# Kernel tuning notes

Measured on AMD Instinct MI355X. Metric: run time of the kernel, lower is better.

Reference implementation:

```python
import jax, jax.numpy as jnp
import numpy as np
import math

# B queries, N complex ambient dim, M codebook entries, S payload dim, K quad nodes
B, N, M, S, K = 1024, 128, 8192, 256, 8
EPS_TOTAL = 1e-3
OVERLAP, ANISO = 0.25, 0.75
_t, _w = np.polynomial.hermite.hermgauss(K)
GH_T = jnp.asarray(_t, jnp.float32)
GH_W = jnp.asarray(_w, jnp.float32)


def _init_sigmas():
    # mirrors CPSFFusedCodebook._init_sigmas (log-space for numerical safety at N=128)
    rho = 1.0 + ANISO
    logV = (N / 2.0) * math.log(math.pi) - math.lgamma(N / 2.0 + 1.0)
    log_r = (math.log(OVERLAP) - math.log(M) - logV - math.log(rho)) / N
    r_perp = math.exp(log_r)
    s_perp = 2.0 * math.pi * r_perp ** 2
    return rho * rho * s_perp, s_perp


def setup_inputs() -> dict:
    key = jax.random.key(0)
    ks = jax.random.split(key, 12)
    u = lambda k, sh: jax.random.uniform(k, sh, jnp.float32, -1.0, 1.0)
    s_par, s_perp = _init_sigmas()
    return {
        "z_re": u(ks[0], (B, N)), "z_im": u(ks[1], (B, N)),
        "d_re": u(ks[2], (B, N)), "d_im": u(ks[3], (B, N)),
        "zj_re": 0.5 * u(ks[4], (M, N)), "zj_im": 0.5 * u(ks[5], (M, N)),
        "dj_re": 0.5 * u(ks[6], (M, N)), "dj_im": 0.5 * u(ks[7], (M, N)),
        "T_re": u(ks[8], (M, S)), "T_im": u(ks[9], (M, S)),
        "alpha": jax.random.uniform(ks[10], (M,), jnp.float32, 0.5, 1.5),
        "sigma_par": jnp.full((M,), s_par, jnp.float32),
        "sigma_perp": jnp.full((M,), s_perp, jnp.float32),
    }


def _unit(xr, xi):
    n = jnp.sqrt(jnp.sum(xr * xr + xi * xi, -1, keepdims=True))
    n = jnp.where(n == 0, jnp.ones_like(n), n)
    return xr / n, xi / n


def _forward(z_re, z_im, d_re, d_im, zj_re, zj_im, dj_re, dj_im,
             T_re, T_im, alpha, sigma_par, sigma_perp):
    tiny = jnp.float32(np.finfo(np.float32).tiny)
    dur, dui = _unit(d_re, d_im)          # autonorm_vec_d
    djr, dji = _unit(dj_re, dj_im)        # autonorm_vec_d_j
    a = jnp.maximum(alpha, tiny)
    sp = jnp.maximum(sigma_par, tiny)
    sq = jnp.maximum(sigma_perp, tiny)

    # proj[b,m] = <d_j, z - z_j> (conj-linear in d_j); all via GEMMs, no [B,M,N] tensor
    pr = z_re @ djr.T + z_im @ dji.T - jnp.sum(djr * zj_re + dji * zj_im, -1)[None, :]
    pi = z_im @ djr.T - z_re @ dji.T - jnp.sum(djr * zj_im - dji * zj_re, -1)[None, :]

    # |z - z_j|^2 via GEMM expansion
    dz2 = (jnp.sum(z_re * z_re + z_im * z_im, -1)[:, None]
           + jnp.sum(zj_re * zj_re + zj_im * zj_im, -1)[None, :]
           - 2.0 * (z_re @ zj_re.T + z_im @ zj_im.T))
    perp2 = jnp.maximum(dz2 - (pr * pr + pi * pi), 0.0)  # component orthogonal to d_j

    # Gauss-Hermite quadrature along the codebook direction, scaled per-code
    scale = jnp.sqrt(sp / jnp.pi)                     # [M]
    t = GH_T[None, :] * scale[:, None]                # [M,K] quad offsets
    par2 = (pr[:, :, None] - t[None]) ** 2 + (pi * pi)[:, :, None]   # [B,M,K]
    env = jnp.exp(-jnp.pi * (par2 / sp[None, :, None]
                             + (perp2 / sq[None, :])[:, :, None]))
    rho = jnp.einsum('bmk,k->bm', env, GH_W) * (scale / jnp.sqrt(jnp.pi))[None, :]

    # angular alignment |<d_j, d>|^2
    ar = dur @ djr.T + dui @ dji.T
    ai = dui @ djr.T - dur @ dji.T
    align = ar * ar + ai * ai

    w = a[None, :] * align * rho                      # [B,M] real mixture weights
    den = jnp.sum(w, -1) + EPS_TOTAL                  # [B]
    out_re = (w @ T_re) / den[:, None]                # [B,S]
    out_im = (w @ T_im) / den[:, None]
    return jnp.stack([out_re, out_im], -1)            # [B,S,2] == complex [B,S]


def reference(z_re, z_im, d_re, d_im, zj_re, zj_im, dj_re, dj_im,
              T_re, T_im, alpha, sigma_par, sigma_perp):
    return _forward(z_re, z_im, d_re, d_im, zj_re, zj_im, dj_re, dj_im,
                    T_re, T_im, alpha, sigma_par, sigma_perp)
```

## Files before the change

### kernel.cpp

```cpp
#include <hip/hip_runtime.h>
#include <math.h>

#define Bq 1024
#define Nn 128
#define Mm 8192
#define Ss 256

typedef _Float16 f16;
typedef _Float16 f16x8 __attribute__((ext_vector_type(8)));
typedef _Float16 f16x4 __attribute__((ext_vector_type(4)));
typedef float f32x4 __attribute__((ext_vector_type(4)));

#define PI_F 3.14159265358979323846f
#define INV_SQRT_PI 0.5641895835477563f
#define TINY_F 1.17549435e-38f
#define EPS_TOTAL 1e-3f
#define WSC 1024.0f

#define GLOAD16(g, l) \
    __builtin_amdgcn_global_load_lds((const __attribute__((address_space(1))) void*)(g), \
                                     (__attribute__((address_space(3))) void*)(l), 16, 0, 0)

__global__ void cpsf_prep_b(const float* __restrict__ z_re, const float* __restrict__ z_im,
                            const float* __restrict__ d_re, const float* __restrict__ d_im,
                            float* __restrict__ z2, float* __restrict__ invd)
{
    const int b = blockIdx.x * 4 + (threadIdx.x >> 6);
    const int l = threadIdx.x & 63;
    const int o = b * Nn;
    float dr0 = d_re[o + l], dr1 = d_re[o + l + 64];
    float di0 = d_im[o + l], di1 = d_im[o + l + 64];
    float zr0 = z_re[o + l], zr1 = z_re[o + l + 64];
    float zi0 = z_im[o + l], zi1 = z_im[o + l + 64];
    float sd = dr0*dr0 + di0*di0 + dr1*dr1 + di1*di1;
    float sz = zr0*zr0 + zi0*zi0 + zr1*zr1 + zi1*zi1;
#pragma unroll
    for (int off = 1; off < 64; off <<= 1) {
        sd += __shfl_xor(sd, off);
        sz += __shfl_xor(sz, off);
    }
    if (l == 0) {
        float nd = sqrtf(sd);
        nd = (nd == 0.0f) ? 1.0f : nd;
        z2[b] = sz;
        invd[b] = 1.0f / nd;
    }
}

__global__ void cpsf_prep_m(const float* __restrict__ zj_re, const float* __restrict__ zj_im,
                            const float* __restrict__ dj_re, const float* __restrict__ dj_im,
                            const float* __restrict__ alpha, const float* __restrict__ sp_,
                            const float* __restrict__ sq_, float* __restrict__ cm)
{
    const int m = blockIdx.x * 4 + (threadIdx.x >> 6);
    const int l = threadIdx.x & 63;
    const int o = m * Nn;
    float dr0 = dj_re[o + l], dr1 = dj_re[o + l + 64];
    float di0 = dj_im[o + l], di1 = dj_im[o + l + 64];
    float zr0 = zj_re[o + l], zr1 = zj_re[o + l + 64];
    float zi0 = zj_im[o + l], zi1 = zj_im[o + l + 64];
    float snd = dr0*dr0 + di0*di0 + dr1*dr1 + di1*di1;
    float sc1 = dr0*zr0 + di0*zi0 + dr1*zr1 + di1*zi1;
    float sc2 = dr0*zi0 - di0*zr0 + dr1*zi1 - di1*zr1;
    float sz2 = zr0*zr0 + zi0*zi0 + zr1*zr1 + zi1*zi1;
#pragma unroll
    for (int off = 1; off < 64; off <<= 1) {
        snd += __shfl_xor(snd, off);
        sc1 += __shfl_xor(sc1, off);
        sc2 += __shfl_xor(sc2, off);
        sz2 += __shfl_xor(sz2, off);
    }
    if (l == 0) {
        float nd = sqrtf(snd);
        nd = (nd == 0.0f) ? 1.0f : nd;
        float inv = 1.0f / nd;
        cm[0*Mm + m] = inv;
        cm[1*Mm + m] = sc1 * inv;
        cm[2*Mm + m] = sc2 * inv;
        cm[3*Mm + m] = sz2;
        float sp = fmaxf(sp_[m], TINY_F);
        float sq = fmaxf(sq_[m], TINY_F);
        float sc = sqrtf(sp / PI_F);
        cm[4*Mm + m] = PI_F / sp;
        cm[5*Mm + m] = PI_F / sq;
        cm[6*Mm + m] = fmaxf(alpha[m], TINY_F) * sc * INV_SQRT_PI;
        cm[7*Mm + m] = sc;
    }
}

__global__ void cpsf_pack_ab(const float* __restrict__ z_re, const float* __restrict__ z_im,
                             const float* __restrict__ d_re, const float* __restrict__ d_im,
                             const float* __restrict__ invd, f16* __restrict__ Az, f16* __restrict__ Au)
{
    int idx = blockIdx.x * 256 + threadIdx.x;
    int b = idx >> 6, k4 = (idx & 63) * 4;
    float4 vz, vd;
    if (k4 < 128) {
        vz = *(const float4*)(z_re + b * Nn + k4);
        vd = *(const float4*)(d_re + b * Nn + k4);
    } else {
        vz = *(const float4*)(z_im + b * Nn + k4 - 128);
        vd = *(const float4*)(d_im + b * Nn + k4 - 128);
    }
    float s = invd[b];
    *(f16x4*)(Az + b * 256 + k4) = (f16x4){(f16)vz.x, (f16)vz.y, (f16)vz.z, (f16)vz.w};
    *(f16x4*)(Au + b * 256 + k4) = (f16x4){(f16)(vd.x*s), (f16)(vd.y*s), (f16)(vd.z*s), (f16)(vd.w*s)};
}

__global__ void cpsf_pack_b1(const float* __restrict__ zj_re, const float* __restrict__ zj_im,
                             const float* __restrict__ dj_re, const float* __restrict__ dj_im,
                             const float* __restrict__ cm, f16* __restrict__ Bp,
                             int Mc, int m0g, int mshift)
{
    int idx = blockIdx.x * 256 + threadIdx.x;
    int r = idx >> 6, k4 = (idx & 63) * 4;
    int p = r >> mshift, ml = r & (Mc - 1);
    int m = m0g + ml;
    float4 v; float s;
    if (p == 0) {
        v = (k4 < 128) ? *(const float4*)(dj_re + m * Nn + k4)
                       : *(const float4*)(dj_im + m * Nn + k4 - 128);
        s = cm[m];
    } else if (p == 1) {
        if (k4 < 128) { v = *(const float4*)(dj_im + m * Nn + k4); v.x=-v.x; v.y=-v.y; v.z=-v.z; v.w=-v.w; }
        else          { v = *(const float4*)(dj_re + m * Nn + k4 - 128); }
        s = cm[m];
    } else {
        v = (k4 < 128) ? *(const float4*)(zj_re + m * Nn + k4)
                       : *(const float4*)(zj_im + m * Nn + k4 - 128);
        s = 1.0f;
    }
    *(f16x4*)(Bp + (size_t)r * 256 + k4) = (f16x4){(f16)(v.x*s), (f16)(v.y*s), (f16)(v.z*s), (f16)(v.w*s)};
}

__global__ void cpsf_pack_tt(const float* __restrict__ T_re, const float* __restrict__ T_im,
                             f16* __restrict__ Tt, int Mc, int m0g)
{
    __shared__ float tr[64][65], ti[64][65];
    const int mb = blockIdx.x * 64, sb = blockIdx.y * 64;
    const int tid = threadIdx.x;
    const int i0 = tid >> 6, j = tid & 63;
#pragma unroll
    for (int it = 0; it < 16; ++it) {
        int i = it * 4 + i0;
        tr[i][j] = T_re[(size_t)(m0g + mb + i) * Ss + sb + j];
        ti[i][j] = T_im[(size_t)(m0g + mb + i) * Ss + sb + j];
    }
    __syncthreads();
#pragma unroll
    for (int it = 0; it < 16; ++it) {
        int jj = it * 4 + i0;
        int sp = (sb + jj) * 2;
        Tt[(size_t)sp * Mc + mb + j]       = (f16)tr[j][jj];
        Tt[(size_t)(sp + 1) * Mc + mb + j] = (f16)ti[j][jj];
    }
}

__global__ __launch_bounds__(256, 2) void cpsf_gemm_w(
    const f16* __restrict__ Az, const f16* __restrict__ Au,
    const f16* __restrict__ Bp, const float* __restrict__ cm,
    const float* __restrict__ z2v, f16* __restrict__ wbuf,
    float* __restrict__ den, int Mc, int m0g)
{
    __shared__ __align__(16) f16 sm[1792 * 8];

    const int tid = threadIdx.x;
    const int wid = tid >> 6;
    const int lane = tid & 63;
    const int q = lane >> 4;
    const int li = lane & 15;
    const int mb0 = blockIdx.x * 64;
    const int bb0 = blockIdx.y * 128;
    const int wb0 = (wid >> 1) * 64;
    const int wm0 = (wid & 1) * 32;

    const f16* gp[7];
    f16* lb[7];
#pragma unroll
    for (int i = 0; i < 7; ++i) {
        int c = i * 4 + wid;
        const f16* src;
        if (c < 8) {
            int g = c >> 1, row = (c & 1) * 64 + lane;
            src = Az + (size_t)(bb0 + row) * 256 + g * 8;
        } else if (c < 16) {
            int c2 = c - 8;
            int g = c2 >> 1, row = (c2 & 1) * 64 + lane;
            src = Au + (size_t)(bb0 + row) * 256 + g * 8;
        } else {
            int c2 = c - 16;
            int g = c2 / 3, p = c2 % 3;
            src = Bp + ((size_t)p * Mc + mb0 + lane) * 256 + g * 8;
        }
        gp[i] = src;
        lb[i] = sm + (size_t)(i * 256 + wid * 64) * 8;
    }

    f32x4 accP[4][2][3];
    f32x4 accQ[4][2][2];
#pragma unroll
    for (int t = 0; t < 4; ++t)
#pragma unroll
        for (int u = 0; u < 2; ++u) {
#pragma unroll
            for (int p = 0; p < 3; ++p) accP[t][u][p] = (f32x4){0.f,0.f,0.f,0.f};
#pragma unroll
            for (int p = 0; p < 2; ++p) accQ[t][u][p] = (f32x4){0.f,0.f,0.f,0.f};
        }

    for (int ks = 0; ks < 8; ++ks) {
        __syncthreads();
#pragma unroll
        for (int i = 0; i < 7; ++i) {
            GLOAD16(gp[i], lb[i]);
            gp[i] += 32;
        }
        __syncthreads();

        f16x8 az[4], au[4], bf[3][2];
#pragma unroll
        for (int t = 0; t < 4; ++t) {
            az[t] = *(const f16x8*)(sm + (size_t)(q * 128 + wb0 + t * 16 + li) * 8);
            au[t] = *(const f16x8*)(sm + (size_t)(512 + q * 128 + wb0 + t * 16 + li) * 8);
        }
#pragma unroll
        for (int p = 0; p < 3; ++p)
#pragma unroll
            for (int u = 0; u < 2; ++u)
                bf[p][u] = *(const f16x8*)(sm + (size_t)(1024 + q * 192 + p * 64 + wm0 + u * 16 + li) * 8);

#pragma unroll
        for (int t = 0; t < 4; ++t)
#pragma unroll
            for (int u = 0; u < 2; ++u) {
#pragma unroll
                for (int p = 0; p < 3; ++p)
                    accP[t][u][p] = __builtin_amdgcn_mfma_f32_16x16x32_f16(az[t], bf[p][u], accP[t][u][p], 0, 0, 0);
#pragma unroll
                for (int p = 0; p < 2; ++p)
                    accQ[t][u][p] = __builtin_amdgcn_mfma_f32_16x16x32_f16(au[t], bf[p][u], accQ[t][u][p], 0, 0, 0);
            }
    }

    const float GT[8] = {-2.9306374202572440f, -1.9816567566958429f,
                         -1.1571937124467802f, -0.3811869902073221f,
                          0.3811869902073221f,  1.1571937124467802f,
                          1.9816567566958429f,  2.9306374202572440f};
    const float GW[8] = {1.9960407221136762e-04f, 1.7077983007413475e-02f,
                         2.0780232581489188e-01f, 6.6114701255824129e-01f,
                         6.6114701255824129e-01f, 2.0780232581489188e-01f,
                         1.7077983007413475e-02f, 1.9960407221136762e-04f};

    float c1[2], c2[2], zj2[2], isp[2], isq[2], cf[2], scl[2];
#pragma unroll
    for (int u = 0; u < 2; ++u) {
        int mg = m0g + mb0 + wm0 + u * 16 + li;
        c1[u]  = cm[1*Mm + mg];  c2[u]  = cm[2*Mm + mg];
        zj2[u] = cm[3*Mm + mg];  isp[u] = cm[4*Mm + mg];
        isq[u] = cm[5*Mm + mg];  cf[u]  = cm[6*Mm + mg];
        scl[u] = cm[7*Mm + mg];
    }

    float dsum[4][4];
#pragma unroll
    for (int t = 0; t < 4; ++t)
#pragma unroll
        for (int r = 0; r < 4; ++r) dsum[t][r] = 0.f;

#pragma unroll
    for (int t = 0; t < 4; ++t) {
#pragma unroll
        for (int r = 0; r < 4; ++r) {
            const int b = bb0 + wb0 + t * 16 + q * 4 + r;
            const float z2b = z2v[b];
#pragma unroll
            for (int u = 0; u < 2; ++u) {
                float pr = accP[t][u][0][r] - c1[u];
                float pi = accP[t][u][1][r] - c2[u];
                float dz2 = z2b + zj2[u] - 2.0f * accP[t][u][2][r];
                float perp2 = fmaxf(dz2 - pr * pr - pi * pi, 0.0f);
                float base = -(isq[u] * perp2 + isp[u] * pi * pi);
                float rho = 0.0f;
#pragma unroll
                for (int k = 0; k < 8; ++k) {
                    float dd = pr - scl[u] * GT[k];
                    rho = fmaf(GW[k], __expf(base - isp[u] * dd * dd), rho);
                }
                float ar = accQ[t][u][0][r], ai = accQ[t][u][1][r];
                float wv = cf[u] * (ar * ar + ai * ai) * rho;
                dsum[t][r] += wv;
                wbuf[(size_t)b * Mc + mb0 + wm0 + u * 16 + li] = (f16)(wv * WSC);
            }
        }
    }
#pragma unroll
    for (int t = 0; t < 4; ++t)
#pragma unroll
        for (int r = 0; r < 4; ++r) {
            float v = dsum[t][r];
            v += __shfl_xor(v, 1);
            v += __shfl_xor(v, 2);
            v += __shfl_xor(v, 4);
            v += __shfl_xor(v, 8);
            if (li == 0) atomicAdd(den + bb0 + wb0 + t * 16 + q * 4 + r, v);
        }
}

__global__ __launch_bounds__(256, 3) void cpsf_gemm_out(
    const f16* __restrict__ wbuf, const f16* __restrict__ Tt,
    float* __restrict__ oacc, int Mc, int Kw)
{
    __shared__ __align__(16) f16 sm[1024 * 8];
    const int tid = threadIdx.x;
    const int wid = tid >> 6;
    const int lane = tid & 63;
    const int q = lane >> 4;
    const int li = lane & 15;
    const int sb0 = blockIdx.x * 128;
    const int bb0 = blockIdx.y * 128;
    const int kz0 = blockIdx.z * Kw;
    const int wb0 = (wid >> 1) * 64;
    const int ws0 = (wid & 1) * 64;

    const f16* gp[4];
    f16* lb[4];
#pragma unroll
    for (int i = 0; i < 4; ++i) {
        int c = i * 4 + wid;
        const f16* src;
        if (c < 8) {
            int g = c >> 1, row = (c & 1) * 64 + lane;
            src = wbuf + (size_t)(bb0 + row) * Mc + kz0 + g * 8;
        } else {
            int c2 = c - 8;
            int g = c2 >> 1, row = (c2 & 1) * 64 + lane;
            src = Tt + (size_t)(sb0 + row) * Mc + kz0 + g * 8;
        }
        gp[i] = src;
        lb[i] = sm + (size_t)(i * 256 + wid * 64) * 8;
    }

    f32x4 acc[4][4];
#pragma unroll
    for (int t = 0; t < 4; ++t)
#pragma unroll
        for (int u = 0; u < 4; ++u) acc[t][u] = (f32x4){0.f,0.f,0.f,0.f};

    for (int kc = 0; kc < Kw; kc += 32) {
        __syncthreads();
#pragma unroll
        for (int i = 0; i < 4; ++i) {
            GLOAD16(gp[i], lb[i]);
            gp[i] += 32;
        }
        __syncthreads();
        f16x8 af[4], bf[4];
#pragma unroll
        for (int t = 0; t < 4; ++t)
            af[t] = *(const f16x8*)(sm + (size_t)(q * 128 + wb0 + t * 16 + li) * 8);
#pragma unroll
        for (int u = 0; u < 4; ++u)
            bf[u] = *(const f16x8*)(sm + (size_t)(512 + q * 128 + ws0 + u * 16 + li) * 8);
#pragma unroll
        for (int t = 0; t < 4; ++t)
#pragma unroll
            for (int u = 0; u < 4; ++u)
                acc[t][u] = __builtin_amdgcn_mfma_f32_16x16x32_f16(af[t], bf[u], acc[t][u], 0, 0, 0);
    }
#pragma unroll
    for (int t = 0; t < 4; ++t)
#pragma unroll
        for (int u = 0; u < 4; ++u)
#pragma unroll
            for (int r = 0; r < 4; ++r)
                atomicAdd(oacc + (size_t)(bb0 + wb0 + t * 16 + q * 4 + r) * 512 + sb0 + ws0 + u * 16 + li,
                          acc[t][u][r]);
}

__global__ void cpsf_fin(const float* __restrict__ oacc, const float* __restrict__ den,
                         float* __restrict__ out)
{
    int i = blockIdx.x * 256 + threadIdx.x;
    float d = (den[i >> 9] + EPS_TOTAL) * WSC;
    out[i] = oacc[i] / d;
}

extern "C" void kernel_launch(void* const* d_in, const int* in_sizes, int n_in,
                              void* d_out, int out_size, void* d_ws, size_t ws_size,
                              hipStream_t stream)
{
    (void)in_sizes; (void)n_in; (void)out_size;
    const float* z_re  = (const float*)d_in[0];
    const float* z_im  = (const float*)d_in[1];
    const float* d_re  = (const float*)d_in[2];
    const float* d_im  = (const float*)d_in[3];
    const float* zj_re = (const float*)d_in[4];
    const float* zj_im = (const float*)d_in[5];
    const float* dj_re = (const float*)d_in[6];
    const float* dj_im = (const float*)d_in[7];
    const float* T_re  = (const float*)d_in[8];
    const float* T_im  = (const float*)d_in[9];
    const float* alpha = (const float*)d_in[10];
    const float* s_par = (const float*)d_in[11];
    const float* s_perp= (const float*)d_in[12];

    char* w8 = (char*)d_ws;
    const size_t o_out  = 0;
    const size_t o_den  = o_out + (size_t)Bq * 512 * 4;
    const size_t o_z2   = o_den + 4096;
    const size_t o_invd = o_z2 + 4096;
    const size_t o_cm   = o_invd + 4096;
    const size_t o_az   = o_cm + (size_t)8 * Mm * 4;
    const size_t o_au   = o_az + (size_t)Bq * 256 * 2;
    const size_t o_ch   = o_au + (size_t)Bq * 256 * 2;
    int Mc = 512;
    if      (o_ch + (size_t)4608 * 8192 <= ws_size) Mc = 8192;
    else if (o_ch + (size_t)4608 * 4096 <= ws_size) Mc = 4096;
    else if (o_ch + (size_t)4608 * 2048 <= ws_size) Mc = 2048;
    else if (o_ch + (size_t)4608 * 1024 <= ws_size) Mc = 1024;
    int mshift = 31 - __builtin_clz((unsigned)Mc);
    int zs = Mc / 1024; if (zs < 1) zs = 1;
    int Kw = Mc / zs;

    float* oacc = (float*)(w8 + o_out);
    float* den  = (float*)(w8 + o_den);
    float* z2   = (float*)(w8 + o_z2);
    float* invd = (float*)(w8 + o_invd);
    float* cm   = (float*)(w8 + o_cm);
    f16*   Az   = (f16*)(w8 + o_az);
    f16*   Au   = (f16*)(w8 + o_au);
    f16*   Bp   = (f16*)(w8 + o_ch);
    f16*   Tt   = (f16*)(w8 + o_ch + (size_t)1536 * Mc);
    f16*   wb   = (f16*)(w8 + o_ch + (size_t)2560 * Mc);

    hipMemsetAsync(d_ws, 0, o_z2, stream);

    cpsf_prep_b<<<Bq / 4, 256, 0, stream>>>(z_re, z_im, d_re, d_im, z2, invd);
    cpsf_prep_m<<<Mm / 4, 256, 0, stream>>>(zj_re, zj_im, dj_re, dj_im, alpha, s_par, s_perp, cm);
    cpsf_pack_ab<<<(Bq * 64) / 256, 256, 0, stream>>>(z_re, z_im, d_re, d_im, invd, Az, Au);

    for (int m0 = 0; m0 < Mm; m0 += Mc) {
        cpsf_pack_b1<<<(3 * Mc * 64) / 256, 256, 0, stream>>>(zj_re, zj_im, dj_re, dj_im,
                                                              cm, Bp, Mc, m0, mshift);
        cpsf_pack_tt<<<dim3(Mc / 64, Ss / 64), 256, 0, stream>>>(T_re, T_im, Tt, Mc, m0);
        cpsf_gemm_w<<<dim3(Mc / 64, Bq / 128), 256, 0, stream>>>(Az, Au, Bp, cm, z2, wb, den, Mc, m0);
        cpsf_gemm_out<<<dim3(4, Bq / 128, zs), 256, 0, stream>>>(wb, Tt, oacc, Mc, Kw);
    }
    cpsf_fin<<<(Bq * 512) / 256, 256, 0, stream>>>(oacc, den, (float*)d_out);
}
```

Before: 247.9 us.

## Split alignment GEMM into separate kernel to shrink gemm_w register pressure

```diff
diff --git a/kernel.cpp b/kernel.cpp
--- a/kernel.cpp
+++ b/kernel.cpp
@@ -156,13 +156,93 @@
     }
 }
 
+__global__ __launch_bounds__(256, 2) void cpsf_align(
+    const f16* __restrict__ Au, const f16* __restrict__ Bp,
+    f16* __restrict__ wbuf, int Mc)
+{
+    __shared__ __align__(16) f16 sm[1536 * 8];
+
+    const int tid = threadIdx.x;
+    const int wid = tid >> 6;
+    const int lane = tid & 63;
+    const int q = lane >> 4;
+    const int li = lane & 15;
+    const int mb0 = blockIdx.x * 128;
+    const int bb0 = blockIdx.y * 128;
+    const int wb0 = (wid >> 1) * 64;
+    const int wm0 = (wid & 1) * 64;
+
+    const f16* gp[6];
+    f16* lb[6];
+#pragma unroll
+    for (int i = 0; i < 6; ++i) {
+        int c = i * 4 + wid;
+        const f16* src;
+        if (c < 8) {
+            int g = c >> 1, row = (c & 1) * 64 + lane;
+            src = Au + (size_t)(bb0 + row) * 256 + g * 8;
+        } else {
+            int c2 = c - 8;
+            int g = c2 >> 2, p = (c2 >> 1) & 1, row = (c2 & 1) * 64 + lane;
+            src = Bp + ((size_t)p * Mc + mb0 + row) * 256 + g * 8;
+        }
+        gp[i] = src;
+        lb[i] = sm + (size_t)(i * 4 + wid) * 64 * 8;
+    }
+
+    f32x4 acc[4][4][2];
+#pragma unroll
+    for (int t = 0; t < 4; ++t)
+#pragma unroll
+        for (int u = 0; u < 4; ++u) {
+            acc[t][u][0] = (f32x4){0.f,0.f,0.f,0.f};
+            acc[t][u][1] = (f32x4){0.f,0.f,0.f,0.f};
+        }
+
+    for (int ks = 0; ks < 8; ++ks) {
+        __syncthreads();
+#pragma unroll
+        for (int i = 0; i < 6; ++i) {
+            GLOAD16(gp[i], lb[i]);
+            gp[i] += 32;
+        }
+        __syncthreads();
+        f16x8 au[4], bf[2][4];
+#pragma unroll
+        for (int t = 0; t < 4; ++t)
+            au[t] = *(const f16x8*)(sm + (size_t)(q * 128 + wb0 + t * 16 + li) * 8);
+#pragma unroll
+        for (int p = 0; p < 2; ++p)
+#pragma unroll
+            for (int u = 0; u < 4; ++u)
+                bf[p][u] = *(const f16x8*)(sm + (size_t)(512 + q * 256 + p * 128 + wm0 + u * 16 + li) * 8);
+#pragma unroll
+        for (int t = 0; t < 4; ++t)
+#pragma unroll
+            for (int u = 0; u < 4; ++u) {
+                acc[t][u][0] = __builtin_amdgcn_mfma_f32_16x16x32_f16(au[t], bf[0][u], acc[t][u][0], 0, 0, 0);
+                acc[t][u][1] = __builtin_amdgcn_mfma_f32_16x16x32_f16(au[t], bf[1][u], acc[t][u][1], 0, 0, 0);
+            }
+    }
+#pragma unroll
+    for (int t = 0; t < 4; ++t)
+#pragma unroll
+        for (int u = 0; u < 4; ++u)
+#pragma unroll
+            for (int r = 0; r < 4; ++r) {
+                int b = bb0 + wb0 + t * 16 + q * 4 + r;
+                int m = mb0 + wm0 + u * 16 + li;
+                float ar = acc[t][u][0][r], ai = acc[t][u][1][r];
+                wbuf[(size_t)b * Mc + m] = (f16)(ar * ar + ai * ai);
+            }
+}
+
 __global__ __launch_bounds__(256, 2) void cpsf_gemm_w(
-    const f16* __restrict__ Az, const f16* __restrict__ Au,
-    const f16* __restrict__ Bp, const float* __restrict__ cm,
-    const float* __restrict__ z2v, f16* __restrict__ wbuf,
-    float* __restrict__ den, int Mc, int m0g)
-{
-    __shared__ __align__(16) f16 sm[1792 * 8];
+    const f16* __restrict__ Az, const f16* __restrict__ Bp,
+    const float* __restrict__ cm, const float* __restrict__ z2v,
+    f16* __restrict__ wbuf, float* __restrict__ den, int Mc, int m0g)
+{
+    __shared__ __align__(16) f16 sm[1280 * 8];
 
     const int tid = threadIdx.x;
     const int wid = tid >> 6;
@@ -174,72 +254,56 @@
     const int wb0 = (wid >> 1) * 64;
     const int wm0 = (wid & 1) * 32;
 
-    const f16* gp[7];
-    f16* lb[7];
-#pragma unroll
-    for (int i = 0; i < 7; ++i) {
+    const f16* gp[5];
+    f16* lb[5];
+#pragma unroll
+    for (int i = 0; i < 5; ++i) {
         int c = i * 4 + wid;
         const f16* src;
         if (c < 8) {
             int g = c >> 1, row = (c & 1) * 64 + lane;
             src = Az + (size_t)(bb0 + row) * 256 + g * 8;
-        } else if (c < 16) {
+        } else {
             int c2 = c - 8;
-            int g = c2 >> 1, row = (c2 & 1) * 64 + lane;
-            src = Au + (size_t)(bb0 + row) * 256 + g * 8;
-        } else {
-            int c2 = c - 16;
             int g = c2 / 3, p = c2 % 3;
             src = Bp + ((size_t)p * Mc + mb0 + lane) * 256 + g * 8;
         }
         gp[i] = src;
-        lb[i] = sm + (size_t)(i * 256 + wid * 64) * 8;
+        lb[i] = sm + (size_t)(i * 4 + wid) * 64 * 8;
     }
 
     f32x4 accP[4][2][3];
-    f32x4 accQ[4][2][2];
-#pragma unroll
-    for (int t = 0; t < 4; ++t)
-#pragma unroll
-        for (int u = 0; u < 2; ++u) {
+#pragma unroll
+    for (int t = 0; t < 4; ++t)
+#pragma unroll
+        for (int u = 0; u < 2; ++u)
 #pragma unroll
             for (int p = 0; p < 3; ++p) accP[t][u][p] = (f32x4){0.f,0.f,0.f,0.f};
-#pragma unroll
-            for (int p = 0; p < 2; ++p) accQ[t][u][p] = (f32x4){0.f,0.f,0.f,0.f};
-        }
 
     for (int ks = 0; ks < 8; ++ks) {
         __syncthreads();
 #pragma unroll
-        for (int i = 0; i < 7; ++i) {
+        for (int i = 0; i < 5; ++i) {
             GLOAD16(gp[i], lb[i]);
             gp[i] += 32;
         }
         __syncthreads();
-
-        f16x8 az[4], au[4], bf[3][2];
-#pragma unroll
-        for (int t = 0; t < 4; ++t) {
+        f16x8 az[4], bf[3][2];
+#pragma unroll
+        for (int t = 0; t < 4; ++t)
             az[t] = *(const f16x8*)(sm + (size_t)(q * 128 + wb0 + t * 16 + li) * 8);
-            au[t] = *(const f16x8*)(sm + (size_t)(512 + q * 128 + wb0 + t * 16 + li) * 8);
-        }
 #pragma unroll
         for (int p = 0; p < 3; ++p)
 #pragma unroll
             for (int u = 0; u < 2; ++u)
-                bf[p][u] = *(const f16x8*)(sm + (size_t)(1024 + q * 192 + p * 64 + wm0 + u * 16 + li) * 8);
-
+                bf[p][u] = *(const f16x8*)(sm + (size_t)(512 + q * 192 + p * 64 + wm0 + u * 16 + li) * 8);
 #pragma unroll
         for (int t = 0; t < 4; ++t)
 #pragma unroll
-            for (int u = 0; u < 2; ++u) {
+            for (int u = 0; u < 2; ++u)
 #pragma unroll
                 for (int p = 0; p < 3; ++p)
                     accP[t][u][p] = __builtin_amdgcn_mfma_f32_16x16x32_f16(az[t], bf[p][u], accP[t][u][p], 0, 0, 0);
-#pragma unroll
-                for (int p = 0; p < 2; ++p)
-                    accQ[t][u][p] = __builtin_amdgcn_mfma_f32_16x16x32_f16(au[t], bf[p][u], accQ[t][u][p], 0, 0, 0);
-            }
     }
 
     const float GT[8] = {-2.9306374202572440f, -1.9816567566958429f,
@@ -275,6 +339,8 @@
             const float z2b = z2v[b];
 #pragma unroll
             for (int u = 0; u < 2; ++u) {
+                const size_t widx = (size_t)b * Mc + mb0 + wm0 + u * 16 + li;
+                float al = (float)wbuf[widx];
                 float pr = accP[t][u][0][r] - c1[u];
                 float pi = accP[t][u][1][r] - c2[u];
                 float dz2 = z2b + zj2[u] - 2.0f * accP[t][u][2][r];
@@ -286,10 +352,9 @@
                     float dd = pr - scl[u] * GT[k];
                     rho = fmaf(GW[k], __expf(base - isp[u] * dd * dd), rho);
                 }
-                float ar = accQ[t][u][0][r], ai = accQ[t][u][1][r];
-                float wv = cf[u] * (ar * ar + ai * ai) * rho;
+                float wv = cf[u] * al * rho;
                 dsum[t][r] += wv;
-                wbuf[(size_t)b * Mc + mb0 + wm0 + u * 16 + li] = (f16)(wv * WSC);
+                wbuf[widx] = (f16)(wv * WSC);
             }
         }
     }
@@ -419,7 +484,7 @@
     else if (o_ch + (size_t)4608 * 2048 <= ws_size) Mc = 2048;
     else if (o_ch + (size_t)4608 * 1024 <= ws_size) Mc = 1024;
     int mshift = 31 - __builtin_clz((unsigned)Mc);
-    int zs = Mc / 1024; if (zs < 1) zs = 1;
+    int zs = Mc / 512; if (zs < 1) zs = 1;
     int Kw = Mc / zs;
 
     float* oacc = (float*)(w8 + o_out);
@@ -443,7 +508,8 @@
         cpsf_pack_b1<<<(3 * Mc * 64) / 256, 256, 0, stream>>>(zj_re, zj_im, dj_re, dj_im,
                                                               cm, Bp, Mc, m0, mshift);
         cpsf_pack_tt<<<dim3(Mc / 64, Ss / 64), 256, 0, stream>>>(T_re, T_im, Tt, Mc, m0);
-        cpsf_gemm_w<<<dim3(Mc / 64, Bq / 128), 256, 0, stream>>>(Az, Au, Bp, cm, z2, wb, den, Mc, m0);
+        cpsf_align<<<dim3(Mc / 128, Bq / 128), 256, 0, stream>>>(Au, Bp, wb, Mc);
+        cpsf_gemm_w<<<dim3(Mc / 64, Bq / 128), 256, 0, stream>>>(Az, Bp, cm, z2, wb, den, Mc, m0);
         cpsf_gemm_out<<<dim3(4, Bq / 128, zs), 256, 0, stream>>>(wb, Tt, oacc, Mc, Kw);
     }
     cpsf_fin<<<(Bq * 512) / 256, 256, 0, stream>>>(oacc, den, (float*)d_out);
```

Measured after the change: 275.0 us. +11.0%, slower.

## Fuse fp16 packing into prep kernels, drop M-chunking, retile both GEMMs

Applied to the files above, without the earlier changes.

```diff
diff --git a/kernel.cpp b/kernel.cpp
--- a/kernel.cpp
+++ b/kernel.cpp
@@ -8,7 +8,6 @@
 
 typedef _Float16 f16;
 typedef _Float16 f16x8 __attribute__((ext_vector_type(8)));
-typedef _Float16 f16x4 __attribute__((ext_vector_type(4)));
 typedef float f32x4 __attribute__((ext_vector_type(4)));
 
 #define PI_F 3.14159265358979323846f
@@ -21,9 +20,9 @@
     __builtin_amdgcn_global_load_lds((const __attribute__((address_space(1))) void*)(g), \
                                      (__attribute__((address_space(3))) void*)(l), 16, 0, 0)
 
-__global__ void cpsf_prep_b(const float* __restrict__ z_re, const float* __restrict__ z_im,
+__global__ void cpsf_prep_a(const float* __restrict__ z_re, const float* __restrict__ z_im,
                             const float* __restrict__ d_re, const float* __restrict__ d_im,
-                            float* __restrict__ z2, float* __restrict__ invd)
+                            float* __restrict__ z2, f16* __restrict__ Az, f16* __restrict__ Au)
 {
     const int b = blockIdx.x * 4 + (threadIdx.x >> 6);
     const int l = threadIdx.x & 63;
@@ -39,18 +38,22 @@
         sd += __shfl_xor(sd, off);
         sz += __shfl_xor(sz, off);
     }
-    if (l == 0) {
-        float nd = sqrtf(sd);
-        nd = (nd == 0.0f) ? 1.0f : nd;
-        z2[b] = sz;
-        invd[b] = 1.0f / nd;
-    }
+    float nd = sqrtf(sd);
+    nd = (nd == 0.0f) ? 1.0f : nd;
+    float inv = 1.0f / nd;
+    if (l == 0) z2[b] = sz;
+    const int o2 = b * 256;
+    Az[o2 + l]       = (f16)zr0;  Az[o2 + 64 + l]  = (f16)zr1;
+    Az[o2 + 128 + l] = (f16)zi0;  Az[o2 + 192 + l] = (f16)zi1;
+    Au[o2 + l]       = (f16)(dr0*inv);  Au[o2 + 64 + l]  = (f16)(dr1*inv);
+    Au[o2 + 128 + l] = (f16)(di0*inv);  Au[o2 + 192 + l] = (f16)(di1*inv);
 }
 
 __global__ void cpsf_prep_m(const float* __restrict__ zj_re, const float* __restrict__ zj_im,
                             const float* __restrict__ dj_re, const float* __restrict__ dj_im,
                             const float* __restrict__ alpha, const float* __restrict__ sp_,
-                            const float* __restrict__ sq_, float* __restrict__ cm)
+                            const float* __restrict__ sq_, float* __restrict__ cm,
+                            f16* __restrict__ Bp)
 {
     const int m = blockIdx.x * 4 + (threadIdx.x >> 6);
     const int l = threadIdx.x & 63;
@@ -70,11 +73,19 @@
         sc2 += __shfl_xor(sc2, off);
         sz2 += __shfl_xor(sz2, off);
     }
+    float nd = sqrtf(snd);
+    nd = (nd == 0.0f) ? 1.0f : nd;
+    float inv = 1.0f / nd;
+    const size_t b0o = (size_t)m * 256;
+    const size_t b1o = ((size_t)Mm + m) * 256;
+    const size_t b2o = ((size_t)2 * Mm + m) * 256;
+    Bp[b0o + l]       = (f16)(dr0*inv);  Bp[b0o + 64 + l]  = (f16)(dr1*inv);
+    Bp[b0o + 128 + l] = (f16)(di0*inv);  Bp[b0o + 192 + l] = (f16)(di1*inv);
+    Bp[b1o + l]       = (f16)(-di0*inv); Bp[b1o + 64 + l]  = (f16)(-di1*inv);
+    Bp[b1o + 128 + l] = (f16)(dr0*inv);  Bp[b1o + 192 + l] = (f16)(dr1*inv);
+    Bp[b2o + l]       = (f16)zr0;        Bp[b2o + 64 + l]  = (f16)zr1;
+    Bp[b2o + 128 + l] = (f16)zi0;        Bp[b2o + 192 + l] = (f16)zi1;
     if (l == 0) {
-        float nd = sqrtf(snd);
-        nd = (nd == 0.0f) ? 1.0f : nd;
-        float inv = 1.0f / nd;
-        cm[0*Mm + m] = inv;
         cm[1*Mm + m] = sc1 * inv;
         cm[2*Mm + m] = sc2 * inv;
         cm[3*Mm + m] = sz2;
@@ -88,53 +99,8 @@
     }
 }
 
-__global__ void cpsf_pack_ab(const float* __restrict__ z_re, const float* __restrict__ z_im,
-                             const float* __restrict__ d_re, const float* __restrict__ d_im,
-                             const float* __restrict__ invd, f16* __restrict__ Az, f16* __restrict__ Au)
-{
-    int idx = blockIdx.x * 256 + threadIdx.x;
-    int b = idx >> 6, k4 = (idx & 63) * 4;
-    float4 vz, vd;
-    if (k4 < 128) {
-        vz = *(const float4*)(z_re + b * Nn + k4);
-        vd = *(const float4*)(d_re + b * Nn + k4);
-    } else {
-        vz = *(const float4*)(z_im + b * Nn + k4 - 128);
-        vd = *(const float4*)(d_im + b * Nn + k4 - 128);
-    }
-    float s = invd[b];
-    *(f16x4*)(Az + b * 256 + k4) = (f16x4){(f16)vz.x, (f16)vz.y, (f16)vz.z, (f16)vz.w};
-    *(f16x4*)(Au + b * 256 + k4) = (f16x4){(f16)(vd.x*s), (f16)(vd.y*s), (f16)(vd.z*s), (f16)(vd.w*s)};
-}
-
-__global__ void cpsf_pack_b1(const float* __restrict__ zj_re, const float* __restrict__ zj_im,
-                             const float* __restrict__ dj_re, const float* __restrict__ dj_im,
-                             const float* __restrict__ cm, f16* __restrict__ Bp,
-                             int Mc, int m0g, int mshift)
-{
-    int idx = blockIdx.x * 256 + threadIdx.x;
-    int r = idx >> 6, k4 = (idx & 63) * 4;
-    int p = r >> mshift, ml = r & (Mc - 1);
-    int m = m0g + ml;
-    float4 v; float s;
-    if (p == 0) {
-        v = (k4 < 128) ? *(const float4*)(dj_re + m * Nn + k4)
-                       : *(const float4*)(dj_im + m * Nn + k4 - 128);
-        s = cm[m];
-    } else if (p == 1) {
-        if (k4 < 128) { v = *(const float4*)(dj_im + m * Nn + k4); v.x=-v.x; v.y=-v.y; v.z=-v.z; v.w=-v.w; }
-        else          { v = *(const float4*)(dj_re + m * Nn + k4 - 128); }
-        s = cm[m];
-    } else {
-        v = (k4 < 128) ? *(const float4*)(zj_re + m * Nn + k4)
-                       : *(const float4*)(zj_im + m * Nn + k4 - 128);
-        s = 1.0f;
-    }
-    *(f16x4*)(Bp + (size_t)r * 256 + k4) = (f16x4){(f16)(v.x*s), (f16)(v.y*s), (f16)(v.z*s), (f16)(v.w*s)};
-}
-
 __global__ void cpsf_pack_tt(const float* __restrict__ T_re, const float* __restrict__ T_im,
-                             f16* __restrict__ Tt, int Mc, int m0g)
+                             f16* __restrict__ Tt)
 {
     __shared__ float tr[64][65], ti[64][65];
     const int mb = blockIdx.x * 64, sb = blockIdx.y * 64;
@@ -143,26 +109,26 @@
 #pragma unroll
     for (int it = 0; it < 16; ++it) {
         int i = it * 4 + i0;
-        tr[i][j] = T_re[(size_t)(m0g + mb + i) * Ss + sb + j];
-        ti[i][j] = T_im[(size_t)(m0g + mb + i) * Ss + sb + j];
+        tr[i][j] = T_re[(size_t)(mb + i) * Ss + sb + j];
+        ti[i][j] = T_im[(size_t)(mb + i) * Ss + sb + j];
     }
     __syncthreads();
 #pragma unroll
     for (int it = 0; it < 16; ++it) {
         int jj = it * 4 + i0;
         int sp = (sb + jj) * 2;
-        Tt[(size_t)sp * Mc + mb + j]       = (f16)tr[j][jj];
-        Tt[(size_t)(sp + 1) * Mc + mb + j] = (f16)ti[j][jj];
-    }
-}
-
-__global__ __launch_bounds__(256, 2) void cpsf_gemm_w(
+        Tt[(size_t)sp * Mm + mb + j]       = (f16)tr[j][jj];
+        Tt[(size_t)(sp + 1) * Mm + mb + j] = (f16)ti[j][jj];
+    }
+}
+
+__global__ __launch_bounds__(256, 3) void cpsf_gemm_w(
     const f16* __restrict__ Az, const f16* __restrict__ Au,
     const f16* __restrict__ Bp, const float* __restrict__ cm,
     const float* __restrict__ z2v, f16* __restrict__ wbuf,
-    float* __restrict__ den, int Mc, int m0g)
-{
-    __shared__ __align__(16) f16 sm[1792 * 8];
+    float* __restrict__ den)
+{
+    __shared__ __align__(16) f16 sm[2560 * 8];
 
     const int tid = threadIdx.x;
     const int wid = tid >> 6;
@@ -170,36 +136,33 @@
     const int q = lane >> 4;
     const int li = lane & 15;
     const int mb0 = blockIdx.x * 64;
-    const int bb0 = blockIdx.y * 128;
-    const int wb0 = (wid >> 1) * 64;
+    const int bb0 = blockIdx.y * 64;
+    const int wb0 = (wid >> 1) * 32;
     const int wm0 = (wid & 1) * 32;
 
-    const f16* gp[7];
-    f16* lb[7];
-#pragma unroll
-    for (int i = 0; i < 7; ++i) {
+    const f16* gp[10];
+    f16* lb[10];
+#pragma unroll
+    for (int i = 0; i < 10; ++i) {
         int c = i * 4 + wid;
         const f16* src;
         if (c < 8) {
-            int g = c >> 1, row = (c & 1) * 64 + lane;
-            src = Az + (size_t)(bb0 + row) * 256 + g * 8;
+            src = Az + (size_t)(bb0 + lane) * 256 + c * 8;
         } else if (c < 16) {
-            int c2 = c - 8;
-            int g = c2 >> 1, row = (c2 & 1) * 64 + lane;
-            src = Au + (size_t)(bb0 + row) * 256 + g * 8;
+            int g = c - 8;
+            src = Au + (size_t)(bb0 + lane) * 256 + g * 8;
         } else {
-            int c2 = c - 16;
-            int g = c2 / 3, p = c2 % 3;
-            src = Bp + ((size_t)p * Mc + mb0 + lane) * 256 + g * 8;
+            int c2 = c - 16, g = c2 / 3, p = c2 % 3;
+            src = Bp + ((size_t)p * Mm + mb0 + lane) * 256 + g * 8;
         }
         gp[i] = src;
-        lb[i] = sm + (size_t)(i * 256 + wid * 64) * 8;
-    }
-
-    f32x4 accP[4][2][3];
-    f32x4 accQ[4][2][2];
-#pragma unroll
-    for (int t = 0; t < 4; ++t)
+        lb[i] = sm + (size_t)c * 64 * 8;
+    }
+
+    f32x4 accP[2][2][3];
+    f32x4 accQ[2][2][2];
+#pragma unroll
+    for (int t = 0; t < 2; ++t)
 #pragma unroll
         for (int u = 0; u < 2; ++u) {
 #pragma unroll
@@ -208,38 +171,39 @@
             for (int p = 0; p < 2; ++p) accQ[t][u][p] = (f32x4){0.f,0.f,0.f,0.f};
         }
 
-    for (int ks = 0; ks < 8; ++ks) {
+    for (int ks = 0; ks < 4; ++ks) {
         __syncthreads();
 #pragma unroll
-        for (int i = 0; i < 7; ++i) {
+        for (int i = 0; i < 10; ++i) {
             GLOAD16(gp[i], lb[i]);
-            gp[i] += 32;
+            gp[i] += 64;
         }
         __syncthreads();
-
-        f16x8 az[4], au[4], bf[3][2];
-#pragma unroll
-        for (int t = 0; t < 4; ++t) {
-            az[t] = *(const f16x8*)(sm + (size_t)(q * 128 + wb0 + t * 16 + li) * 8);
-            au[t] = *(const f16x8*)(sm + (size_t)(512 + q * 128 + wb0 + t * 16 + li) * 8);
-        }
-#pragma unroll
-        for (int p = 0; p < 3; ++p)
-#pragma unroll
-            for (int u = 0; u < 2; ++u)
-                bf[p][u] = *(const f16x8*)(sm + (size_t)(1024 + q * 192 + p * 64 + wm0 + u * 16 + li) * 8);
-
-#pragma unroll
-        for (int t = 0; t < 4; ++t)
-#pragma unroll
-            for (int u = 0; u < 2; ++u) {
-#pragma unroll
-                for (int p = 0; p < 3; ++p)
-                    accP[t][u][p] = __builtin_amdgcn_mfma_f32_16x16x32_f16(az[t], bf[p][u], accP[t][u][p], 0, 0, 0);
-#pragma unroll
-                for (int p = 0; p < 2; ++p)
-                    accQ[t][u][p] = __builtin_amdgcn_mfma_f32_16x16x32_f16(au[t], bf[p][u], accQ[t][u][p], 0, 0, 0);
+#pragma unroll
+        for (int j = 0; j < 2; ++j) {
+            const int g = j * 4 + q;
+            f16x8 az[2], au[2], bf[3][2];
+#pragma unroll
+            for (int t = 0; t < 2; ++t) {
+                az[t] = *(const f16x8*)(sm + (size_t)(g * 64 + wb0 + t * 16 + li) * 8);
+                au[t] = *(const f16x8*)(sm + (size_t)(512 + g * 64 + wb0 + t * 16 + li) * 8);
             }
+#pragma unroll
+            for (int p = 0; p < 3; ++p)
+#pragma unroll
+                for (int u = 0; u < 2; ++u)
+                    bf[p][u] = *(const f16x8*)(sm + (size_t)(1024 + (g * 3 + p) * 64 + wm0 + u * 16 + li) * 8);
+#pragma unroll
+            for (int t = 0; t < 2; ++t)
+#pragma unroll
+                for (int u = 0; u < 2; ++u) {
+#pragma unroll
+                    for (int p = 0; p < 3; ++p)
+                        accP[t][u][p] = __builtin_amdgcn_mfma_f32_16x16x32_f16(az[t], bf[p][u], accP[t][u][p], 0, 0, 0);
+                    accQ[t][u][0] = __builtin_amdgcn_mfma_f32_16x16x32_f16(au[t], bf[0][u], accQ[t][u][0], 0, 0, 0);
+                    accQ[t][u][1] = __builtin_amdgcn_mfma_f32_16x16x32_f16(au[t], bf[1][u], accQ[t][u][1], 0, 0, 0);
+                }
+        }
     }
 
     const float GT[8] = {-2.9306374202572440f, -1.9816567566958429f,
@@ -254,21 +218,21 @@
     float c1[2], c2[2], zj2[2], isp[2], isq[2], cf[2], scl[2];
 #pragma unroll
     for (int u = 0; u < 2; ++u) {
-        int mg = m0g + mb0 + wm0 + u * 16 + li;
+        int mg = mb0 + wm0 + u * 16 + li;
         c1[u]  = cm[1*Mm + mg];  c2[u]  = cm[2*Mm + mg];
         zj2[u] = cm[3*Mm + mg];  isp[u] = cm[4*Mm + mg];
         isq[u] = cm[5*Mm + mg];  cf[u]  = cm[6*Mm + mg];
         scl[u] = cm[7*Mm + mg];
     }
 
-    float dsum[4][4];
-#pragma unroll
-    for (int t = 0; t < 4; ++t)
+    float dsum[2][4];
+#pragma unroll
+    for (int t = 0; t < 2; ++t)
 #pragma unroll
         for (int r = 0; r < 4; ++r) dsum[t][r] = 0.f;
 
 #pragma unroll
-    for (int t = 0; t < 4; ++t) {
+    for (int t = 0; t < 2; ++t) {
 #pragma unroll
         for (int r = 0; r < 4; ++r) {
             const int b = bb0 + wb0 + t * 16 + q * 4 + r;
@@ -289,12 +253,12 @@
                 float ar = accQ[t][u][0][r], ai = accQ[t][u][1][r];
                 float wv = cf[u] * (ar * ar + ai * ai) * rho;
                 dsum[t][r] += wv;
-                wbuf[(size_t)b * Mc + mb0 + wm0 + u * 16 + li] = (f16)(wv * WSC);
+                wbuf[(size_t)b * Mm + mb0 + wm0 + u * 16 + li] = (f16)(wv * WSC);
             }
         }
     }
 #pragma unroll
-    for (int t = 0; t < 4; ++t)
+    for (int t = 0; t < 2; ++t)
 #pragma unroll
         for (int r = 0; r < 4; ++r) {
             float v = dsum[t][r];
@@ -306,69 +270,74 @@
         }
 }
 
-__global__ __launch_bounds__(256, 3) void cpsf_gemm_out(
+__global__ __launch_bounds__(256, 4) void cpsf_gemm_out(
     const f16* __restrict__ wbuf, const f16* __restrict__ Tt,
-    float* __restrict__ oacc, int Mc, int Kw)
-{
-    __shared__ __align__(16) f16 sm[1024 * 8];
+    float* __restrict__ oacc)
+{
+    __shared__ __align__(16) f16 sm[1536 * 8];
     const int tid = threadIdx.x;
     const int wid = tid >> 6;
     const int lane = tid & 63;
     const int q = lane >> 4;
     const int li = lane & 15;
     const int sb0 = blockIdx.x * 128;
-    const int bb0 = blockIdx.y * 128;
-    const int kz0 = blockIdx.z * Kw;
-    const int wb0 = (wid >> 1) * 64;
+    const int bb0 = blockIdx.y * 64;
+    const int kz0 = blockIdx.z * 1024;
+    const int wb0 = (wid >> 1) * 32;
     const int ws0 = (wid & 1) * 64;
 
-    const f16* gp[4];
-    f16* lb[4];
-#pragma unroll
-    for (int i = 0; i < 4; ++i) {
+    const f16* gp[6];
+    f16* lb[6];
+#pragma unroll
+    for (int i = 0; i < 6; ++i) {
         int c = i * 4 + wid;
         const f16* src;
+        f16* dst;
         if (c < 8) {
-            int g = c >> 1, row = (c & 1) * 64 + lane;
-            src = wbuf + (size_t)(bb0 + row) * Mc + kz0 + g * 8;
+            src = wbuf + (size_t)(bb0 + lane) * Mm + kz0 + c * 8;
+            dst = sm + (size_t)c * 64 * 8;
         } else {
-            int c2 = c - 8;
-            int g = c2 >> 1, row = (c2 & 1) * 64 + lane;
-            src = Tt + (size_t)(sb0 + row) * Mc + kz0 + g * 8;
+            int c2 = c - 8, g = c2 >> 1, rh = c2 & 1;
+            src = Tt + (size_t)(sb0 + rh * 64 + lane) * Mm + kz0 + g * 8;
+            dst = sm + (size_t)(512 + g * 128 + rh * 64) * 8;
         }
         gp[i] = src;
-        lb[i] = sm + (size_t)(i * 256 + wid * 64) * 8;
-    }
-
-    f32x4 acc[4][4];
-#pragma unroll
-    for (int t = 0; t < 4; ++t)
+        lb[i] = dst;
+    }
+
+    f32x4 acc[2][4];
+#pragma unroll
+    for (int t = 0; t < 2; ++t)
 #pragma unroll
         for (int u = 0; u < 4; ++u) acc[t][u] = (f32x4){0.f,0.f,0.f,0.f};
 
-    for (int kc = 0; kc < Kw; kc += 32) {
+    for (int ks = 0; ks < 16; ++ks) {
         __syncthreads();
 #pragma unroll
-        for (int i = 0; i < 4; ++i) {
+        for (int i = 0; i < 6; ++i) {
             GLOAD16(gp[i], lb[i]);
-            gp[i] += 32;
+            gp[i] += 64;
         }
         __syncthreads();
-        f16x8 af[4], bf[4];
-#pragma unroll
-        for (int t = 0; t < 4; ++t)
-            af[t] = *(const f16x8*)(sm + (size_t)(q * 128 + wb0 + t * 16 + li) * 8);
-#pragma unroll
-        for (int u = 0; u < 4; ++u)
-            bf[u] = *(const f16x8*)(sm + (size_t)(512 + q * 128 + ws0 + u * 16 + li) * 8);
-#pragma unroll
-        for (int t = 0; t < 4; ++t)
+#pragma unroll
+        for (int j = 0; j < 2; ++j) {
+            const int g = j * 4 + q;
+            f16x8 af[2], bf[4];
+#pragma unroll
+            for (int t = 0; t < 2; ++t)
+                af[t] = *(const f16x8*)(sm + (size_t)(g * 64 + wb0 + t * 16 + li) * 8);
 #pragma unroll
             for (int u = 0; u < 4; ++u)
-                acc[t][u] = __builtin_amdgcn_mfma_f32_16x16x32_f16(af[t], bf[u], acc[t][u], 0, 0, 0);
-    }
-#pragma unroll
-    for (int t = 0; t < 4; ++t)
+                bf[u] = *(const f16x8*)(sm + (size_t)(512 + g * 128 + ws0 + u * 16 + li) * 8);
+#pragma unroll
+            for (int t = 0; t < 2; ++t)
+#pragma unroll
+                for (int u = 0; u < 4; ++u)
+                    acc[t][u] = __builtin_amdgcn_mfma_f32_16x16x32_f16(af[t], bf[u], acc[t][u], 0, 0, 0);
+        }
+    }
+#pragma unroll
+    for (int t = 0; t < 2; ++t)
 #pragma unroll
         for (int u = 0; u < 4; ++u)
 #pragma unroll
@@ -389,7 +358,7 @@
                               void* d_out, int out_size, void* d_ws, size_t ws_size,
                               hipStream_t stream)
 {
-    (void)in_sizes; (void)n_in; (void)out_size;
+    (void)in_sizes; (void)n_in; (void)out_size; (void)ws_size;
     const float* z_re  = (const float*)d_in[0];
     const float* z_im  = (const float*)d_in[1];
     const float* d_re  = (const float*)d_in[2];
@@ -405,46 +374,33 @@
     const float* s_perp= (const float*)d_in[12];
 
     char* w8 = (char*)d_ws;
-    const size_t o_out  = 0;
-    const size_t o_den  = o_out + (size_t)Bq * 512 * 4;
-    const size_t o_z2   = o_den + 4096;
-    const size_t o_invd = o_z2 + 4096;
-    const size_t o_cm   = o_invd + 4096;
-    const size_t o_az   = o_cm + (size_t)8 * Mm * 4;
-    const size_t o_au   = o_az + (size_t)Bq * 256 * 2;
-    const size_t o_ch   = o_au + (size_t)Bq * 256 * 2;
-    int Mc = 512;
-    if      (o_ch + (size_t)4608 * 8192 <= ws_size) Mc = 8192;
-    else if (o_ch + (size_t)4608 * 4096 <= ws_size) Mc = 4096;
-    else if (o_ch + (size_t)4608 * 2048 <= ws_size) Mc = 2048;
-    else if (o_ch + (size_t)4608 * 1024 <= ws_size) Mc = 1024;
-    int mshift = 31 - __builtin_clz((unsigned)Mc);
-    int zs = Mc / 1024; if (zs < 1) zs = 1;
-    int Kw = Mc / zs;
+    const size_t o_out = 0;
+    const size_t o_den = o_out + (size_t)Bq * 512 * 4;
+    const size_t o_z2  = o_den + 4096;
+    const size_t o_cm  = o_z2 + 4096;
+    const size_t o_az  = o_cm + (size_t)8 * Mm * 4;
+    const size_t o_au  = o_az + (size_t)Bq * 256 * 2;
+    const size_t o_bp  = o_au + (size_t)Bq * 256 * 2;
+    const size_t o_tt  = o_bp + (size_t)3 * Mm * 256 * 2;
+    const size_t o_wb  = o_tt + (size_t)512 * Mm * 2;
 
     float* oacc = (float*)(w8 + o_out);
     float* den  = (float*)(w8 + o_den);
     float* z2   = (float*)(w8 + o_z2);
-    float* invd = (float*)(w8 + o_invd);
     float* cm   = (float*)(w8 + o_cm);
     f16*   Az   = (f16*)(w8 + o_az);
     f16*   Au   = (f16*)(w8 + o_au);
-    f16*   Bp   = (f16*)(w8 + o_ch);
-    f16*   Tt   = (f16*)(w8 + o_ch + (size_t)1536 * Mc);
-    f16*   wb   = (f16*)(w8 + o_ch + (size_t)2560 * Mc);
-
-    hipMemsetAsync(d_ws, 0, o_z2, stream);
-
-    cpsf_prep_b<<<Bq / 4, 256, 0, stream>>>(z_re, z_im, d_re, d_im, z2, invd);
-    cpsf_prep_m<<<Mm / 4, 256, 0, stream>>>(zj_re, zj_im, dj_re, dj_im, alpha, s_par, s_perp, cm);
-    cpsf_pack_ab<<<(Bq * 64) / 256, 256, 0, stream>>>(z_re, z_im, d_re, d_im, invd, Az, Au);
-
-    for (int m0 = 0; m0 < Mm; m0 += Mc) {
-        cpsf_pack_b1<<<(3 * Mc * 64) / 256, 256, 0, stream>>>(zj_re, zj_im, dj_re, dj_im,
-                                                              cm, Bp, Mc, m0, mshift);
-        cpsf_pack_tt<<<dim3(Mc / 64, Ss / 64), 256, 0, stream>>>(T_re, T_im, Tt, Mc, m0);
-        cpsf_gemm_w<<<dim3(Mc / 64, Bq / 128), 256, 0, stream>>>(Az, Au, Bp, cm, z2, wb, den, Mc, m0);
-        cpsf_gemm_out<<<dim3(4, Bq / 128, zs), 256, 0, stream>>>(wb, Tt, oacc, Mc, Kw);
-    }
+    f16*   Bp   = (f16*)(w8 + o_bp);
+    f16*   Tt   = (f16*)(w8 + o_tt);
+    f16*   wb   = (f16*)(w8 + o_wb);
+
+    hipMemsetAsync(d_ws, 0, o_cm, stream);
+
+    cpsf_prep_a<<<Bq / 4, 256, 0, stream>>>(z_re, z_im, d_re, d_im, z2, Az, Au);
+    cpsf_prep_m<<<Mm / 4, 256, 0, stream>>>(zj_re, zj_im, dj_re, dj_im,
+                                            alpha, s_par, s_perp, cm, Bp);
+    cpsf_pack_tt<<<dim3(Mm / 64, Ss / 64), 256, 0, stream>>>(T_re, T_im, Tt);
+    cpsf_gemm_w<<<dim3(Mm / 64, Bq / 64), 256, 0, stream>>>(Az, Au, Bp, cm, z2, wb, den);
+    cpsf_gemm_out<<<dim3(4, Bq / 64, Mm / 1024), 256, 0, stream>>>(wb, Tt, oacc);
     cpsf_fin<<<(Bq * 512) / 256, 256, 0, stream>>>(oacc, den, (float*)d_out);
 }
```

Result: slower. 253.9 us (+2.4%).
